# Kernel tuning notes

Measured on AMD Instinct MI355X. Metric: run time of the kernel, lower is better.

## Reference

```python
import jax, jax.numpy as jnp
import numpy as np

N_NODES = 100000
N_EDGES = 6_400_000
IN_DIM = 128


def gcn_conv(x, W, b, row, col, ew):
    """PyG GCNConv(normalize=True, add_self_loops=True) forward."""
    n = x.shape[0]
    loop = jnp.arange(n)
    row_sl = jnp.concatenate([row, loop])
    col_sl = jnp.concatenate([col, loop])
    ew_sl = jnp.concatenate([ew, jnp.ones((n,), ew.dtype)])
    # symmetric normalization: deg^{-1/2}[src] * w * deg^{-1/2}[dst]
    deg = jax.ops.segment_sum(ew_sl, col_sl, num_segments=n)
    safe_deg = jnp.where(deg > 0, deg, 1.0)
    dis = jnp.where(deg > 0, jax.lax.rsqrt(safe_deg), 0.0)
    norm = dis[row_sl] * ew_sl * dis[col_sl]
    h = x @ W  # [n, out_dim] linear transform first (small out_dim)
    # gather source features, scale, scatter-add into targets
    out = jax.ops.segment_sum(norm[:, None] * h[row_sl], col_sl, num_segments=n)
    return out + b


def setup_inputs() -> dict:
    key = jax.random.key(0)
    ks = jax.random.split(key, 12)
    X = jax.random.normal(ks[0], (N_NODES, IN_DIM), dtype=jnp.float32)
    edge_index = jax.random.randint(ks[1], (2, N_EDGES), 0, N_NODES, dtype=jnp.int64)
    edge_weight = jax.random.uniform(ks[2], (N_EDGES,), dtype=jnp.float32)

    def glorot(k, fan_in, fan_out):
        lim = np.sqrt(6.0 / (fan_in + fan_out)).astype(np.float32)
        return jax.random.uniform(k, (fan_in, fan_out), minval=-lim, maxval=lim, dtype=jnp.float32)

    return {
        "X": X,
        "edge_index": edge_index,
        "edge_weight": edge_weight,
        "W1": glorot(ks[3], IN_DIM, 12), "b1": jnp.zeros((12,), jnp.float32),
        "W2": glorot(ks[4], 12, 6), "b2": jnp.zeros((6,), jnp.float32),
        "W3": glorot(ks[5], 6, 3), "b3": jnp.zeros((3,), jnp.float32),
        "Wl": glorot(ks[6], 3, 1), "bl": jnp.zeros((1,), jnp.float32),
    }


def reference(X, edge_index, edge_weight, W1, b1, W2, b2, W3, b3, Wl, bl):
    row, col = edge_index[0], edge_index[1]
    h = jax.nn.relu(gcn_conv(X, W1, b1, row, col, edge_weight))
    # dropout p=0.2 is identity in eval mode
    h = jax.nn.relu(gcn_conv(h, W2, b2, row, col, edge_weight))
    h = jax.nn.relu(gcn_conv(h, W3, b3, row, col, edge_weight))
    out = jax.nn.sigmoid(h @ Wl + bl)
    return out.squeeze(1)  # [N]
```

## Files before the change

kernel.cpp:

```cpp
#include <hip/hip_runtime.h>
#include <cstdint>
#include <cstddef>

#define RANGE    128
#define RSHIFT   7
#define MAXBUCK  800
#define CSHIFT   12
#define CRANGE   4096
#define MAXC     32
#define FPB      32
#define CH_CNT   8192
#define CH_SC    4096
#define EPT      16
#define PAD      16
#define WSTR     132
#define STAGE_CAP 9216

typedef _Float16 h8 __attribute__((ext_vector_type(8)));

__global__ void zero_pad_kernel(int* __restrict__ p, int n) {
    int i = blockIdx.x * blockDim.x + threadIdx.x;
    if (i < n) p[i * PAD] = 0;
}

__global__ void count_kernel(const int* __restrict__ col, int* __restrict__ fcnt,
                             int nfine, int E) {
    __shared__ int lcnt[MAXBUCK];
    int tid = threadIdx.x;
    for (int i = tid; i < nfine; i += blockDim.x) lcnt[i] = 0;
    __syncthreads();
    int base = blockIdx.x * CH_CNT;
    int end  = min(E, base + CH_CNT);
    for (int e = base + tid; e < end; e += blockDim.x)
        atomicAdd(&lcnt[col[e] >> RSHIFT], 1);
    __syncthreads();
    for (int i = tid; i < nfine; i += blockDim.x)
        if (lcnt[i]) atomicAdd(&fcnt[i * PAD], lcnt[i]);
}

__global__ void scan_kernel(const int* __restrict__ fcnt, int* __restrict__ fbase,
                            int* __restrict__ fcur, int* __restrict__ cbase,
                            int* __restrict__ ccur, int* __restrict__ row_ptr,
                            int nfine, int ncoarse, int N, int E) {
    __shared__ int lds[1024];
    int T = threadIdx.x;
    int s = (T < nfine) ? fcnt[T * PAD] : 0;
    lds[T] = s;
    __syncthreads();
    for (int off = 1; off < 1024; off <<= 1) {
        int v = (T >= off) ? lds[T - off] : 0;
        __syncthreads();
        lds[T] += v;
        __syncthreads();
    }
    int excl = lds[T] - s;
    if (T < nfine) { fbase[T] = excl; fcur[T * PAD] = excl; }
    if ((T & (FPB - 1)) == 0 && (T >> 5) < ncoarse) {
        cbase[T >> 5] = excl;
        ccur[(T >> 5) * PAD] = excl;
    }
    if (T == 0) { fbase[nfine] = E; cbase[ncoarse] = E; row_ptr[N] = E; }
}

__global__ void coarse_scatter_kernel(const int* __restrict__ row, const int* __restrict__ col,
                                      const float* __restrict__ ew, int* __restrict__ ccur,
                                      uint2* __restrict__ partA, int ncoarse, int E) {
    __shared__ uint2 stage[CH_SC];
    __shared__ unsigned char sb[CH_SC];
    __shared__ int lcnt[MAXC], lofs[MAXC], gofs[MAXC];
    __shared__ int total_s;
    int tid = threadIdx.x;
    if (tid < MAXC) lcnt[tid] = 0;
    __syncthreads();
    int base = blockIdx.x * CH_SC;
    int cnt  = min(E - base, CH_SC);

    uint2 rec[EPT]; int rnk[EPT]; int bb[EPT];
#pragma unroll
    for (int k = 0; k < EPT; k++) {
        int idx = tid + (k << 8);
        if (idx < cnt) {
            int e = base + idx;
            int c = col[e];
            int b = c >> CSHIFT;
            bb[k]  = b;
            rec[k] = make_uint2((unsigned)row[e] | ((unsigned)(c & (CRANGE - 1)) << 17),
                                __float_as_uint(ew[e]));
            rnk[k] = atomicAdd(&lcnt[b], 1);
        }
    }
    __syncthreads();
    if (tid == 0) {
        int run = 0;
        for (int i = 0; i < ncoarse; i++) { lofs[i] = run; run += lcnt[i]; }
        total_s = run;
    }
    __syncthreads();
    if (tid < ncoarse) {
        int c = lcnt[tid];
        if (c) {
            int g = atomicAdd(&ccur[tid * PAD], c);
            gofs[tid] = g - lofs[tid];
        }
    }
#pragma unroll
    for (int k = 0; k < EPT; k++) {
        int idx = tid + (k << 8);
        if (idx < cnt) {
            int p = lofs[bb[k]] + rnk[k];
            stage[p] = rec[k];
            sb[p] = (unsigned char)bb[k];
        }
    }
    __syncthreads();
    int total = total_s;
    for (int i = tid; i < total; i += 256)
        partA[gofs[sb[i]] + i] = stage[i];
}

__global__ __launch_bounds__(256, 3)
void fine_scatter_kernel(const uint2* __restrict__ partA, const int* __restrict__ cbase,
                                    int* __restrict__ fcur, uint2* __restrict__ partB,
                                    int nfine, int ncoarse, int E) {
    __shared__ uint2 stage[CH_SC];
    __shared__ unsigned short sb[CH_SC];
    __shared__ int lcnt[MAXBUCK], lofs[MAXBUCK], gofs[MAXBUCK];
    __shared__ int tmp[256];
    __shared__ int scb[MAXC + 1];
    __shared__ int rlo_s, total_s;
    int tid = threadIdx.x;
    int base = blockIdx.x * CH_SC;
    int cnt  = min(E - base, CH_SC);
    if (tid <= ncoarse) scb[tid] = cbase[tid];
    for (int i = tid; i < nfine; i += 256) lcnt[i] = 0;
    if (tid == 0) {
        int r = 0;
        while (r < ncoarse - 1 && cbase[r + 1] <= base) ++r;
        rlo_s = r;
    }
    __syncthreads();
    int rlo = rlo_s;

    uint2 rec[EPT]; int rnk[EPT]; int ff[EPT];
#pragma unroll
    for (int k = 0; k < EPT; k++) {
        int idx = tid + (k << 8);
        if (idx < cnt) {
            int e = base + idx;
            uint2 v = partA[e];
            int r = rlo;
            while (e >= scb[r + 1]) ++r;
            int col12 = (int)((v.x >> 17) & (CRANGE - 1));
            int f = (r << 5) | (col12 >> RSHIFT);
            ff[k]  = f;
            rec[k] = make_uint2((v.x & 0x1FFFFu) | ((unsigned)(col12 & (RANGE - 1)) << 17), v.y);
            rnk[k] = atomicAdd(&lcnt[f], 1);
        }
    }
    __syncthreads();
    {
        const int Cc = (nfine + 255) >> 8;
        int b0 = tid * Cc;
        int s = 0;
        for (int i = 0; i < Cc; i++) {
            int idx = b0 + i;
            if (idx < nfine) s += lcnt[idx];
        }
        tmp[tid] = s;
        __syncthreads();
        for (int off = 1; off < 256; off <<= 1) {
            int v = (tid >= off) ? tmp[tid - off] : 0;
            __syncthreads();
            tmp[tid] += v;
            __syncthreads();
        }
        int run = tmp[tid] - s;
        for (int i = 0; i < Cc; i++) {
            int idx = b0 + i;
            if (idx < nfine) { lofs[idx] = run; run += lcnt[idx]; }
        }
        if (tid == 255) total_s = tmp[255];
    }
    __syncthreads();
    for (int i = tid; i < nfine; i += 256) {
        int c = lcnt[i];
        if (c) {
            int g = atomicAdd(&fcur[i * PAD], c);
            gofs[i] = g - lofs[i];
        }
    }
#pragma unroll
    for (int k = 0; k < EPT; k++) {
        int idx = tid + (k << 8);
        if (idx < cnt) {
            int p = lofs[ff[k]] + rnk[k];
            stage[p] = rec[k];
            sb[p] = (unsigned short)ff[k];
        }
    }
    __syncthreads();
    int total = total_s;
    for (int i = tid; i < total; i += 256)
        partB[gofs[sb[i]] + i] = stage[i];
}

__global__ __launch_bounds__(512, 4)
void bucket_csr_kernel(const uint2* __restrict__ part, const int* __restrict__ bbase,
                       int* __restrict__ row_ptr, float* __restrict__ dis,
                       uint2* __restrict__ csr, int N) {
    extern __shared__ uint2 stage[];
    __shared__ int   scnt[RANGE];
    __shared__ int   sscan[RANGE];
    __shared__ float sdeg[RANGE];
    __shared__ float sdis[RANGE];
    int b = blockIdx.x, tid = threadIdx.x;
    int s = bbase[b], t = bbase[b + 1];
    if (tid < RANGE) { scnt[tid] = 0; sdeg[tid] = 1.0f; }
    __syncthreads();
    for (int e = s + tid; e < t; e += blockDim.x) {
        uint2 r = part[e];
        int c = (r.x >> 17) & (RANGE - 1);
        atomicAdd(&scnt[c], 1);
        atomicAdd(&sdeg[c], __uint_as_float(r.y));
    }
    __syncthreads();
    int cnt_t = 0;
    if (tid < RANGE) { cnt_t = scnt[tid]; sscan[tid] = cnt_t; }
    __syncthreads();
    for (int off = 1; off < RANGE; off <<= 1) {
        int v = 0;
        if (tid < RANGE && tid >= off) v = sscan[tid - off];
        __syncthreads();
        if (tid < RANGE) sscan[tid] += v;
        __syncthreads();
    }
    if (tid < RANGE) {
        int excl = sscan[tid] - cnt_t;
        int node = b * RANGE + tid;
        float dn = rsqrtf(sdeg[tid]);
        sdis[tid] = dn;
        if (node < N) {
            row_ptr[node] = s + excl;
            dis[node] = dn;
        }
        scnt[tid] = excl;
    }
    __syncthreads();
    for (int e = s + tid; e < t; e += blockDim.x) {
        uint2 r = part[e];
        int c   = (r.x >> 17) & (RANGE - 1);
        int src = (int)(r.x & 0x1FFFFu);
        float v = sdis[c] * __uint_as_float(r.y);
        int off = atomicAdd(&scnt[c], 1);
        uint2 rec = make_uint2((unsigned)src, __float_as_uint(v));
        if (off < STAGE_CAP) stage[off] = rec;
        else                 csr[s + off] = rec;
    }
    __syncthreads();
    int lim = min(t - s, STAGE_CAP);
    for (int i = tid; i < lim; i += blockDim.x)
        csr[s + i] = stage[i];
}

__global__ void lin1_kernel(const float* __restrict__ X, const float* __restrict__ W1,
                            const float* __restrict__ dis, uint4* __restrict__ t1, int n) {
    __shared__ float w1t[12 * WSTR];
    int tid = threadIdx.x;
    for (int i = tid; i < 128 * 12; i += 256) {
        int k = i / 12, o = i - k * 12;
        w1t[o * WSTR + k] = W1[i];
    }
    __syncthreads();
    int gt   = blockIdx.x * 256 + tid;
    int node = gt >> 3;
    int sub  = gt & 7;
    if (node >= n) return;

    const float4* xp = (const float4*)(X + (size_t)node * 128 + sub * 16);
    float4 x0 = xp[0], x1 = xp[1], x2 = xp[2], x3 = xp[3];

    float res[12];
#pragma unroll
    for (int o = 0; o < 12; o++) {
        const float4* wp = (const float4*)(w1t + o * WSTR + sub * 16);
        float4 w0 = wp[0], w1v = wp[1], w2 = wp[2], w3 = wp[3];
        float s;
        s  = x0.x * w0.x + x0.y * w0.y + x0.z * w0.z + x0.w * w0.w;
        s += x1.x * w1v.x + x1.y * w1v.y + x1.z * w1v.z + x1.w * w1v.w;
        s += x2.x * w2.x + x2.y * w2.y + x2.z * w2.z + x2.w * w2.w;
        s += x3.x * w3.x + x3.y * w3.y + x3.z * w3.z + x3.w * w3.w;
        res[o] = s;
    }
#pragma unroll
    for (int o = 0; o < 12; o++) {
        res[o] += __shfl_xor(res[o], 1, 64);
        res[o] += __shfl_xor(res[o], 2, 64);
        res[o] += __shfl_xor(res[o], 4, 64);
    }
    if (sub == 0) {
        h8 a, b;
#pragma unroll
        for (int o = 0; o < 8; o++) a[o] = (_Float16)res[o];
#pragma unroll
        for (int o = 0; o < 4; o++) b[o] = (_Float16)res[8 + o];
#pragma unroll
        for (int o = 4; o < 8; o++) b[o] = (_Float16)0.f;
        uint4 ua = __builtin_bit_cast(uint4, a);
        uint4 ub = __builtin_bit_cast(uint4, b);
        ub.z = __float_as_uint(dis[node]);
        ub.w = 0u;
        uint4* dst = t1 + (size_t)node * 2;
        dst[0] = ua;
        dst[1] = ub;
    }
}

template <int DIN, int ROWW, int DOUT, bool LAST>
__global__ void agg_kernel(const int* __restrict__ row_ptr, const uint2* __restrict__ csr,
                           const uint4* __restrict__ hin,
                           const float* __restrict__ b_this, const float* __restrict__ W_next,
                           const float* __restrict__ b_next, void* __restrict__ hout_v, int n) {
    int gt   = blockIdx.x * blockDim.x + threadIdx.x;
    int node = gt >> 3;
    int sub  = gt & 7;
    if (node >= n) return;
    int start = row_ptr[node];
    int end   = row_ptr[node + 1];
    float acc[DIN];
#pragma unroll
    for (int d = 0; d < DIN; d++) acc[d] = 0.f;

    for (int e = start + sub; e < end; e += 8) {
        unsigned long long raw =
            __builtin_nontemporal_load((const unsigned long long*)(csr + e));
        int src    = (int)(unsigned)raw;
        float ewdd = __uint_as_float((unsigned)(raw >> 32));
        const uint4* hr = hin + (size_t)src * ROWW;
        if constexpr (DIN == 12) {
            uint4 ua = hr[0], ub = hr[1];
            float norm = ewdd * __uint_as_float(ub.z);
            h8 a = __builtin_bit_cast(h8, ua);
            h8 b = __builtin_bit_cast(h8, ub);
#pragma unroll
            for (int d = 0; d < 8; d++) acc[d] += norm * (float)a[d];
#pragma unroll
            for (int d = 0; d < 4; d++) acc[8 + d] += norm * (float)b[d];
        } else if constexpr (DIN == 6) {
            uint4 u = hr[0];
            float norm = ewdd * __uint_as_float(u.w);
            h8 a = __builtin_bit_cast(h8, u);
#pragma unroll
            for (int d = 0; d < 6; d++) acc[d] += norm * (float)a[d];
        } else {
            uint4 u = hr[0];
            float norm = ewdd * __uint_as_float(u.z);
            h8 a = __builtin_bit_cast(h8, u);
#pragma unroll
            for (int d = 0; d < 3; d++) acc[d] += norm * (float)a[d];
        }
    }

#pragma unroll
    for (int d = 0; d < DIN; d++) {
        acc[d] += __shfl_xor(acc[d], 1, 64);
        acc[d] += __shfl_xor(acc[d], 2, 64);
        acc[d] += __shfl_xor(acc[d], 4, 64);
    }

    if (sub == 0) {
        const uint4* hn = hin + (size_t)node * ROWW;
        float v[DIN];
        float dn;
        if constexpr (DIN == 12) {
            uint4 ua = hn[0], ub = hn[1];
            dn = __uint_as_float(ub.z);
            float s2 = dn * dn;
            h8 a = __builtin_bit_cast(h8, ua);
            h8 b = __builtin_bit_cast(h8, ub);
#pragma unroll
            for (int d = 0; d < 8; d++) v[d] = fmaxf(acc[d] + s2 * (float)a[d] + b_this[d], 0.f);
#pragma unroll
            for (int d = 0; d < 4; d++) v[8 + d] = fmaxf(acc[8 + d] + s2 * (float)b[d] + b_this[8 + d], 0.f);
        } else if constexpr (DIN == 6) {
            uint4 u = hn[0];
            dn = __uint_as_float(u.w);
            float s2 = dn * dn;
            h8 a = __builtin_bit_cast(h8, u);
#pragma unroll
            for (int d = 0; d < 6; d++) v[d] = fmaxf(acc[d] + s2 * (float)a[d] + b_this[d], 0.f);
        } else {
            uint4 u = hn[0];
            dn = __uint_as_float(u.z);
            float s2 = dn * dn;
            h8 a = __builtin_bit_cast(h8, u);
#pragma unroll
            for (int d = 0; d < 3; d++) v[d] = fmaxf(acc[d] + s2 * (float)a[d] + b_this[d], 0.f);
        }
        if constexpr (!LAST) {
            float o[DOUT];
#pragma unroll
            for (int oo = 0; oo < DOUT; oo++) {
                float z = 0.f;
#pragma unroll
                for (int d = 0; d < DIN; d++) z += v[d] * W_next[d * DOUT + oo];
                o[oo] = z;
            }
            h8 w;
#pragma unroll
            for (int oo = 0; oo < 8; oo++) w[oo] = (_Float16)0.f;
#pragma unroll
            for (int oo = 0; oo < DOUT; oo++) w[oo] = (_Float16)o[oo];
            uint4 uw = __builtin_bit_cast(uint4, w);
            if constexpr (DOUT == 6) uw.w = __float_as_uint(dn);
            else                     uw.z = __float_as_uint(dn);
            ((uint4*)hout_v)[node] = uw;
        } else {
            float z = b_next[0];
#pragma unroll
            for (int d = 0; d < DIN; d++) z += v[d] * W_next[d];
            ((float*)hout_v)[node] = 1.0f / (1.0f + expf(-z));
        }
    }
}

extern "C" void kernel_launch(void* const* d_in, const int* in_sizes, int n_in,
                              void* d_out, int out_size, void* d_ws, size_t ws_size,
                              hipStream_t stream) {
    const float* X  = (const float*)d_in[0];
    const int*   ei = (const int*)d_in[1];
    const float* ew = (const float*)d_in[2];
    const float* W1 = (const float*)d_in[3];
    const float* b1 = (const float*)d_in[4];
    const float* W2 = (const float*)d_in[5];
    const float* b2 = (const float*)d_in[6];
    const float* W3 = (const float*)d_in[7];
    const float* b3 = (const float*)d_in[8];
    const float* Wl = (const float*)d_in[9];
    const float* bl = (const float*)d_in[10];
    float* out = (float*)d_out;

    const int N = in_sizes[0] / 128;
    const int E = in_sizes[1] / 2;
    const int* row = ei;
    const int* col = ei + E;
    const int nfine   = (N + RANGE - 1) >> RSHIFT;
    const int ncoarse = (N + CRANGE - 1) >> CSHIFT;

    char* ws = (char*)d_ws;
    size_t off = 0;
    auto carve = [&](size_t bytes) -> void* {
        void* p = ws + off;
        off += (bytes + 255) & ~(size_t)255;
        return p;
    };
    int*   fcnt    = (int*)  carve((size_t)MAXBUCK * PAD * 4);
    int*   fcur    = (int*)  carve((size_t)MAXBUCK * PAD * 4);
    int*   ccur    = (int*)  carve((size_t)MAXC * PAD * 4);
    int*   cbase   = (int*)  carve((size_t)(MAXC + 1) * 4);
    int*   fbase   = (int*)  carve((size_t)(MAXBUCK + 1) * 4);
    int*   row_ptr = (int*)  carve((size_t)(N + 1) * 4);
    float* dis     = (float*)carve((size_t)N * 4);
    uint2* partA   = (uint2*)carve((size_t)E * 8);
    uint2* partB   = (uint2*)carve((size_t)E * 8);
    uint2* csr = partA;
    uint4* t1  = (uint4*)partB;
    uint4* t2  = t1 + (size_t)N * 2;
    uint4* t3  = t2 + (size_t)N;
    (void)ws_size; (void)n_in; (void)out_size;

    const int bCnt = (E + CH_CNT - 1) / CH_CNT;
    const int bSc  = (E + CH_SC - 1) / CH_SC;
    const int bL   = ((size_t)N * 8 + 255) / 256;
    const int bA   = ((size_t)N * 8 + 255) / 256;

    zero_pad_kernel<<<(nfine + 255) / 256, 256, 0, stream>>>(fcnt, nfine);
    count_kernel<<<bCnt, 256, 0, stream>>>(col, fcnt, nfine, E);
    scan_kernel<<<1, 1024, 0, stream>>>(fcnt, fbase, fcur, cbase, ccur, row_ptr,
                                        nfine, ncoarse, N, E);
    coarse_scatter_kernel<<<bSc, 256, 0, stream>>>(row, col, ew, ccur, partA, ncoarse, E);
    fine_scatter_kernel<<<bSc, 256, 0, stream>>>(partA, cbase, fcur, partB, nfine, ncoarse, E);
    bucket_csr_kernel<<<nfine, 512, (size_t)STAGE_CAP * sizeof(uint2), stream>>>(
        partB, fbase, row_ptr, dis, csr, N);
    lin1_kernel<<<bL, 256, 0, stream>>>(X, W1, dis, t1, N);
    agg_kernel<12, 2, 6, false><<<bA, 256, 0, stream>>>(row_ptr, csr, t1, b1, W2, nullptr, t2, N);
    agg_kernel< 6, 1, 3, false><<<bA, 256, 0, stream>>>(row_ptr, csr, t2, b2, W3, nullptr, t3, N);
    agg_kernel< 3, 1, 1, true ><<<bA, 256, 0, stream>>>(row_ptr, csr, t3, b3, Wl, bl, out, N);
}
```

Before: 545.3 us.

## Stage bucket records in LDS once and unroll aggregation loop by two

```diff
diff --git a/kernel.cpp b/kernel.cpp
--- a/kernel.cpp
+++ b/kernel.cpp
@@ -15,6 +15,7 @@
 #define PAD      16
 #define WSTR     132
 #define STAGE_CAP 9216
+#define KMAX     18
 
 typedef _Float16 h8 __attribute__((ext_vector_type(8)));
 
@@ -215,10 +216,12 @@
     __shared__ float sdis[RANGE];
     int b = blockIdx.x, tid = threadIdx.x;
     int s = bbase[b], t = bbase[b + 1];
+    int cnt = t - s;
     if (tid < RANGE) { scnt[tid] = 0; sdeg[tid] = 1.0f; }
     __syncthreads();
-    for (int e = s + tid; e < t; e += blockDim.x) {
-        uint2 r = part[e];
+    for (int idx = tid; idx < cnt; idx += 512) {
+        uint2 r = part[s + idx];
+        if (idx < STAGE_CAP) stage[idx] = r;
         int c = (r.x >> 17) & (RANGE - 1);
         atomicAdd(&scnt[c], 1);
         atomicAdd(&sdeg[c], __uint_as_float(r.y));
@@ -246,20 +249,38 @@
         scnt[tid] = excl;
     }
     __syncthreads();
-    for (int e = s + tid; e < t; e += blockDim.x) {
-        uint2 r = part[e];
-        int c   = (r.x >> 17) & (RANGE - 1);
-        int src = (int)(r.x & 0x1FFFFu);
-        float v = sdis[c] * __uint_as_float(r.y);
-        int off = atomicAdd(&scnt[c], 1);
-        uint2 rec = make_uint2((unsigned)src, __float_as_uint(v));
-        if (off < STAGE_CAP) stage[off] = rec;
-        else                 csr[s + off] = rec;
-    }
-    __syncthreads();
-    int lim = min(t - s, STAGE_CAP);
-    for (int i = tid; i < lim; i += blockDim.x)
-        csr[s + i] = stage[i];
+
+    if (cnt <= STAGE_CAP) {
+        uint2 rc[KMAX]; int rp[KMAX];
+#pragma unroll
+        for (int k = 0; k < KMAX; k++) {
+            int idx = tid + k * 512;
+            if (idx < cnt) {
+                uint2 r = stage[idx];
+                int c   = (r.x >> 17) & (RANGE - 1);
+                float v = sdis[c] * __uint_as_float(r.y);
+                rp[k] = atomicAdd(&scnt[c], 1);
+                rc[k] = make_uint2(r.x & 0x1FFFFu, __float_as_uint(v));
+            }
+        }
+        __syncthreads();
+#pragma unroll
+        for (int k = 0; k < KMAX; k++) {
+            int idx = tid + k * 512;
+            if (idx < cnt) stage[rp[k]] = rc[k];
+        }
+        __syncthreads();
+        for (int i = tid; i < cnt; i += 512)
+            csr[s + i] = stage[i];
+    } else {
+        for (int idx = tid; idx < cnt; idx += 512) {
+            uint2 r = (idx < STAGE_CAP) ? stage[idx] : part[s + idx];
+            int c   = (r.x >> 17) & (RANGE - 1);
+            float v = sdis[c] * __uint_as_float(r.y);
+            int off = atomicAdd(&scnt[c], 1);
+            csr[s + off] = make_uint2(r.x & 0x1FFFFu, __float_as_uint(v));
+        }
+    }
 }
 
 __global__ void lin1_kernel(const float* __restrict__ X, const float* __restrict__ W1,
@@ -326,13 +347,11 @@
     if (node >= n) return;
     int start = row_ptr[node];
     int end   = row_ptr[node + 1];
-    float acc[DIN];
-#pragma unroll
-    for (int d = 0; d < DIN; d++) acc[d] = 0.f;
-
-    for (int e = start + sub; e < end; e += 8) {
-        unsigned long long raw =
-            __builtin_nontemporal_load((const unsigned long long*)(csr + e));
+    float acc[DIN], acc2[DIN];
+#pragma unroll
+    for (int d = 0; d < DIN; d++) { acc[d] = 0.f; acc2[d] = 0.f; }
+
+    auto body = [&](unsigned long long raw, float* a_) {
         int src    = (int)(unsigned)raw;
         float ewdd = __uint_as_float((unsigned)(raw >> 32));
         const uint4* hr = hin + (size_t)src * ROWW;
@@ -342,26 +361,42 @@
             h8 a = __builtin_bit_cast(h8, ua);
             h8 b = __builtin_bit_cast(h8, ub);
 #pragma unroll
-            for (int d = 0; d < 8; d++) acc[d] += norm * (float)a[d];
-#pragma unroll
-            for (int d = 0; d < 4; d++) acc[8 + d] += norm * (float)b[d];
+            for (int d = 0; d < 8; d++) a_[d] += norm * (float)a[d];
+#pragma unroll
+            for (int d = 0; d < 4; d++) a_[8 + d] += norm * (float)b[d];
         } else if constexpr (DIN == 6) {
             uint4 u = hr[0];
             float norm = ewdd * __uint_as_float(u.w);
             h8 a = __builtin_bit_cast(h8, u);
 #pragma unroll
-            for (int d = 0; d < 6; d++) acc[d] += norm * (float)a[d];
+            for (int d = 0; d < 6; d++) a_[d] += norm * (float)a[d];
         } else {
             uint4 u = hr[0];
             float norm = ewdd * __uint_as_float(u.z);
             h8 a = __builtin_bit_cast(h8, u);
 #pragma unroll
-            for (int d = 0; d < 3; d++) acc[d] += norm * (float)a[d];
-        }
+            for (int d = 0; d < 3; d++) a_[d] += norm * (float)a[d];
+        }
+    };
+
+    int e = start + sub;
+    for (; e + 8 < end; e += 16) {
+        unsigned long long raw0 =
+            __builtin_nontemporal_load((const unsigned long long*)(csr + e));
+        unsigned long long raw1 =
+            __builtin_nontemporal_load((const unsigned long long*)(csr + e + 8));
+        body(raw0, acc);
+        body(raw1, acc2);
+    }
+    if (e < end) {
+        unsigned long long raw0 =
+            __builtin_nontemporal_load((const unsigned long long*)(csr + e));
+        body(raw0, acc);
     }
 
 #pragma unroll
     for (int d = 0; d < DIN; d++) {
+        acc[d] += acc2[d];
         acc[d] += __shfl_xor(acc[d], 1, 64);
         acc[d] += __shfl_xor(acc[d], 2, 64);
         acc[d] += __shfl_xor(acc[d], 4, 64);
```

Result: faster. 515.7 us (-5.4%).
